# Kernel optimization log

Measured on AMD Instinct MI355X. Metric: run time of the kernel, lower is better.

## Reference

```python
import jax, jax.numpy as jnp
import numpy as np

NUM_USERS = 1_000_000
EMBED = 64
BATCH = 16384
DEG = 50


def setup_inputs() -> dict:
    key = jax.random.key(0)
    ks = jax.random.split(key, 7)
    return {
        "nodes": jax.random.randint(ks[0], (BATCH,), 0, NUM_USERS),
        "neighbors": jax.random.randint(ks[1], (BATCH, DEG), 0, NUM_USERS),
        "u_to_e": jax.random.normal(ks[2], (NUM_USERS, EMBED), jnp.float32) * 0.02,
        "w1": jax.random.normal(ks[3], (2 * EMBED, EMBED), jnp.float32) / np.sqrt(2 * EMBED),
        "b1": jnp.zeros((EMBED,), jnp.float32),
        "w2": jax.random.normal(ks[4], (EMBED, EMBED), jnp.float32) / np.sqrt(EMBED),
        "b2": jnp.zeros((EMBED,), jnp.float32),
        "w3": jax.random.normal(ks[5], (EMBED, 1), jnp.float32) / np.sqrt(EMBED),
        "b3": jnp.zeros((1,), jnp.float32),
    }


def reference(nodes, neighbors, u_to_e, w1, b1, w2, b2, w3, b3):
    # Gather self and neighbor embeddings
    e_u = u_to_e[nodes]            # [B, d]
    e_n = u_to_e[neighbors]        # [B, D, d]
    # GraphRec attention MLP on [neighbor_embed ; self_embed]
    x = jnp.concatenate(
        [e_n, jnp.broadcast_to(e_u[:, None, :], e_n.shape)], axis=-1
    )                              # [B, D, 2d]
    h = jax.nn.relu(x @ w1 + b1)   # [B, D, d]  (dropout is identity in eval)
    h = jax.nn.relu(h @ w2 + b2)   # [B, D, d]
    scores = (h @ w3 + b3)[..., 0] # [B, D]
    att = jax.nn.softmax(scores, axis=1)          # softmax over neighbors
    return jnp.einsum("bd,bde->be", att, e_n)      # attention-weighted neighbor sum [B, d]
```

## Files before the change

### kernel.cpp

```cpp
#include <hip/hip_runtime.h>
#include <hip/hip_bf16.h>
#include <stdint.h>


#define BATCH 16384
#define DEG 50

typedef __attribute__((ext_vector_type(8))) short short8;
typedef __attribute__((ext_vector_type(4))) float f32x4;

__device__ __forceinline__ short bf(float f) {
    __hip_bfloat16 h = __float2bfloat16(f);
    return *reinterpret_cast<short*>(&h);
}
__device__ __forceinline__ unsigned pk2(float a, float b) {
    union { unsigned u; unsigned short s[2]; } v;
    v.s[0] = (unsigned short)bf(a);
    v.s[1] = (unsigned short)bf(b);
    return v.u;
}
__device__ __forceinline__ float bf2f(short s) {
    union { float f; unsigned u; } v;
    v.u = (unsigned)(unsigned short)s << 16;
    return v.f;
}
__device__ __forceinline__ short8 pkrow(f32x4 a, f32x4 c) {
    union { short8 s; unsigned u[4]; } v;
    v.u[0] = pk2(a[0], a[1]); v.u[1] = pk2(a[2], a[3]);
    v.u[2] = pk2(c[0], c[1]); v.u[3] = pk2(c[2], c[3]);
    return v.s;
}
__device__ __forceinline__ short8 cvt_row8(const float* p) {
    f32x4 a = *reinterpret_cast<const f32x4*>(p);
    f32x4 c = *reinterpret_cast<const f32x4*>(p + 4);
    return pkrow(a, c);
}

__global__ void pack_weights(const float* __restrict__ w1, const float* __restrict__ w2,
                             short8* __restrict__ ws) {
    const int f = blockIdx.x;
    const int lane = threadIdx.x;
    const int q = lane >> 4, r = lane & 15;
    const float* w = (f < 16) ? w1 : w2;
    const int g  = (f < 16) ? f : (f - 16);
    const int kt = g >> 2, t = g & 3;
    short8 s;
    #pragma unroll
    for (int j = 0; j < 8; ++j)
        s[j] = bf(w[(32*kt + 8*q + j)*64 + 16*t + r]);
    ws[f*64 + lane] = s;
}

__global__ __launch_bounds__(256, 3)
void graphrec_fused(const int* __restrict__ nodes, const int* __restrict__ neighbors,
                    const float* __restrict__ u_to_e,
                    const short8* __restrict__ wpk,
                    const float* __restrict__ b1, const float* __restrict__ b2,
                    const float* __restrict__ w3,
                    float* __restrict__ out)
{
    __shared__ short8 lds_a[24][64];
    __shared__ int    lds_nbr[4][64];
    __shared__ unsigned short lds_h1[4][1024];
    __shared__ float  lds_stage[4][2][512];

    const int tid  = threadIdx.x;
    const int lane = tid & 63;
    const int wid  = tid >> 6;
    const int q    = lane >> 4;
    const int r    = lane & 15;

    #pragma unroll
    for (int i = 0; i < 6; ++i)
        reinterpret_cast<short8*>(lds_a)[tid + 256*i] = wpk[tid + 256*i];

    const int b    = blockIdx.x * 4 + wid;
    const int node = nodes[b];
    lds_nbr[wid][lane] = (lane < DEG) ? neighbors[b * DEG + lane] : 0;
    __syncthreads();

    int rowv[4];
    #pragma unroll
    for (int mt = 0; mt < 4; ++mt) rowv[mt] = lds_nbr[wid][16*mt + r];

    f32x4 cu[4];
    {
        const float* ub = u_to_e + (size_t)node * 64;
        short8 xu0 = cvt_row8(ub + 8*q);
        short8 xu1 = cvt_row8(ub + 32 + 8*q);
        #pragma unroll
        for (int t = 0; t < 4; ++t) {
            cu[t] = *reinterpret_cast<const f32x4*>(b1 + 16*t + 4*q);
            cu[t] = __builtin_amdgcn_mfma_f32_16x16x32_bf16(lds_a[8  + t][lane], xu0, cu[t], 0, 0, 0);
            cu[t] = __builtin_amdgcn_mfma_f32_16x16x32_bf16(lds_a[12 + t][lane], xu1, cu[t], 0, 0, 0);
        }
    }
    f32x4 b2v[4], w3v[4];
    #pragma unroll
    for (int t = 0; t < 4; ++t) {
        b2v[t] = *reinterpret_cast<const f32x4*>(b2 + 16*t + 4*q);
        w3v[t] = *reinterpret_cast<const f32x4*>(w3 + 16*t + 4*q);
    }

    float* stg = &lds_stage[wid][0][0];
    #define ISSUE_HALF(H) do {                                                           \
        const float* base_ = u_to_e + (size_t)rowv[(H) >> 1] * 64 + 32*((H) & 1) + 4*q;  \
        float* dst_ = stg + ((H) & 1) * 512;                                             \
        _Pragma("unroll")                                                                \
        for (int c_ = 0; c_ < 2; ++c_)                                                   \
            __builtin_amdgcn_global_load_lds(                                            \
                (const __attribute__((address_space(1))) void*)(base_ + 16*c_),          \
                (__attribute__((address_space(3))) void*)(dst_ + 256*c_), 16, 0, 0);     \
    } while (0)

    __builtin_amdgcn_sched_barrier(0);
    ISSUE_HALF(0);
    ISSUE_HALF(1);
    __builtin_amdgcn_sched_barrier(0);

    unsigned short* h1base = lds_h1[wid];
    float agg[16];
    #pragma unroll
    for (int i = 0; i < 16; ++i) agg[i] = 0.f;
    float m_run = -INFINITY, s_run = 0.f;
    const int boff = 256*(q >> 1) + 128*(q & 1) + 4*r;

    #pragma unroll
    for (int mt = 0; mt < 4; ++mt) {
        if (mt < 3) asm volatile("s_waitcnt vmcnt(2)" ::: "memory");
        else        asm volatile("s_waitcnt vmcnt(2)" ::: "memory");
        __builtin_amdgcn_sched_barrier(0);
        f32x4 A  = *reinterpret_cast<const f32x4*>(stg + boff);
        f32x4 Bv = *reinterpret_cast<const f32x4*>(stg + boff + 64);
        short8 xf0 = pkrow(A, Bv);
        if (mt < 3) { ISSUE_HALF(2*mt + 2); }

        if (mt < 3) asm volatile("s_waitcnt vmcnt(2)" ::: "memory");
        else        asm volatile("s_waitcnt vmcnt(0)" ::: "memory");
        __builtin_amdgcn_sched_barrier(0);
        f32x4 C  = *reinterpret_cast<const f32x4*>(stg + 512 + boff);
        f32x4 Dv = *reinterpret_cast<const f32x4*>(stg + 512 + boff + 64);
        short8 xf1 = pkrow(C, Dv);
        if (mt < 3) { ISSUE_HALF(2*mt + 3); }

        f32x4 acc[4] = { cu[0], cu[1], cu[2], cu[3] };
        #pragma unroll
        for (int t = 0; t < 4; ++t) {
            acc[t] = __builtin_amdgcn_mfma_f32_16x16x32_bf16(lds_a[t][lane],     xf0, acc[t], 0, 0, 0);
            acc[t] = __builtin_amdgcn_mfma_f32_16x16x32_bf16(lds_a[4 + t][lane], xf1, acc[t], 0, 0, 0);
        }

        #pragma unroll
        for (int t = 0; t < 4; ++t) {
            unsigned lo = pk2(fmaxf(acc[t][0], 0.f), fmaxf(acc[t][1], 0.f));
            unsigned hi = pk2(fmaxf(acc[t][2], 0.f), fmaxf(acc[t][3], 0.f));
            int off = r * 128 + (((16*t + 4*q) * 2) ^ ((r & 7) << 4));
            *reinterpret_cast<uint2*>((char*)h1base + off) = make_uint2(lo, hi);
        }
        f32x4 acc2[4];
        #pragma unroll
        for (int t2 = 0; t2 < 4; ++t2) acc2[t2] = (f32x4){0.f, 0.f, 0.f, 0.f};
        #pragma unroll
        for (int kt2 = 0; kt2 < 2; ++kt2) {
            int roff = r * 128 + (((32*kt2 + 8*q) * 2) ^ ((r & 7) << 4));
            short8 b2f = *reinterpret_cast<const short8*>((const char*)h1base + roff);
            #pragma unroll
            for (int t2 = 0; t2 < 4; ++t2)
                acc2[t2] = __builtin_amdgcn_mfma_f32_16x16x32_bf16(lds_a[16 + kt2*4 + t2][lane], b2f, acc2[t2], 0, 0, 0);
        }
        float sp = 0.f;
        #pragma unroll
        for (int t2 = 0; t2 < 4; ++t2)
            #pragma unroll
            for (int reg = 0; reg < 4; ++reg)
                sp += fmaxf(acc2[t2][reg] + b2v[t2][reg], 0.f) * w3v[t2][reg];
        sp += __shfl_xor(sp, 16, 64);
        sp += __shfl_xor(sp, 32, 64);

        float v = (mt < 3 || r < 2) ? sp : -INFINITY;
        float tm = v;
        tm = fmaxf(tm, __shfl_xor(tm, 1, 64));
        tm = fmaxf(tm, __shfl_xor(tm, 2, 64));
        tm = fmaxf(tm, __shfl_xor(tm, 4, 64));
        tm = fmaxf(tm, __shfl_xor(tm, 8, 64));
        float m_new = fmaxf(m_run, tm);
        float scale = __expf(m_run - m_new);
        float w = __expf(v - m_new);
        s_run = s_run * scale + w;
        #pragma unroll
        for (int kt = 0; kt < 2; ++kt)
            #pragma unroll
            for (int j = 0; j < 8; ++j) {
                float e = bf2f((kt == 0) ? xf0[j] : xf1[j]);
                agg[kt*8 + j] = fmaf(agg[kt*8 + j], scale, w * e);
            }
        m_run = m_new;
    }
    #undef ISSUE_HALF

    float sum = s_run;
    sum += __shfl_xor(sum, 1, 64);
    sum += __shfl_xor(sum, 2, 64);
    sum += __shfl_xor(sum, 4, 64);
    sum += __shfl_xor(sum, 8, 64);
    float inv = 1.f / sum;
    #pragma unroll
    for (int i = 0; i < 16; ++i) agg[i] *= inv;
    #pragma unroll
    for (int d = 1; d < 16; d <<= 1)
        #pragma unroll
        for (int i = 0; i < 16; ++i)
            agg[i] += __shfl_xor(agg[i], d, 64);

    if (r == 0) {
        float* ob = out + (size_t)b * 64;
        *reinterpret_cast<f32x4*>(ob + 8*q)          = (f32x4){ agg[0],  agg[1],  agg[2],  agg[3]  };
        *reinterpret_cast<f32x4*>(ob + 8*q + 4)      = (f32x4){ agg[4],  agg[5],  agg[6],  agg[7]  };
        *reinterpret_cast<f32x4*>(ob + 32 + 8*q)     = (f32x4){ agg[8],  agg[9],  agg[10], agg[11] };
        *reinterpret_cast<f32x4*>(ob + 32 + 8*q + 4) = (f32x4){ agg[12], agg[13], agg[14], agg[15] };
    }
}

extern "C" void kernel_launch(void* const* d_in, const int* in_sizes, int n_in,
                              void* d_out, int out_size, void* d_ws, size_t ws_size,
                              hipStream_t stream) {
    const int*   nodes     = (const int*)d_in[0];
    const int*   neighbors = (const int*)d_in[1];
    const float* u_to_e    = (const float*)d_in[2];
    const float* w1        = (const float*)d_in[3];
    const float* b1        = (const float*)d_in[4];
    const float* w2        = (const float*)d_in[5];
    const float* b2        = (const float*)d_in[6];
    const float* w3        = (const float*)d_in[7];

    pack_weights<<<dim3(24), dim3(64), 0, stream>>>(w1, w2, (short8*)d_ws);
    graphrec_fused<<<dim3(BATCH / 4), dim3(256), 0, stream>>>(
        nodes, neighbors, u_to_e, (const short8*)d_ws, b1, b2, w3, (float*)d_out);
}
```

Measured before the change: 63.02 us.

## Triple-buffer neighbor staging and drop self-embedding weights from LDS

Neighbor embedding halves are now staged through three LDS slots instead of two, so three global-to-LDS loads are in flight ahead of use rather than two. The wait counts are adjusted to match. To make room, the W1 self-embedding fragments, which are used only once, are read straight from global memory and no longer copied into LDS, shrinking the weight area from 24 to 16 fragments. This deepens memory prefetch to hide gather latency, at the cost of an extra vmcnt(0) wait before the first issues and one-off global weight reads.

```diff
diff --git a/kernel.cpp b/kernel.cpp
--- a/kernel.cpp
+++ b/kernel.cpp
@@ -59,10 +59,10 @@
                     const float* __restrict__ w3,
                     float* __restrict__ out)
 {
-    __shared__ short8 lds_a[24][64];
+    __shared__ short8 lds_a[16][64];
     __shared__ int    lds_nbr[4][64];
     __shared__ unsigned short lds_h1[4][1024];
-    __shared__ float  lds_stage[4][2][512];
+    __shared__ float  lds_stage[4][3][512];
 
     const int tid  = threadIdx.x;
     const int lane = tid & 63;
@@ -71,8 +71,11 @@
     const int r    = lane & 15;
 
     #pragma unroll
-    for (int i = 0; i < 6; ++i)
-        reinterpret_cast<short8*>(lds_a)[tid + 256*i] = wpk[tid + 256*i];
+    for (int i = 0; i < 4; ++i) {
+        const int idx = tid + 256*i;
+        const int f = idx >> 6, l = idx & 63;
+        reinterpret_cast<short8*>(lds_a)[idx] = wpk[((f < 8) ? f : (f + 8))*64 + l];
+    }
 
     const int b    = blockIdx.x * 4 + wid;
     const int node = nodes[b];
@@ -91,8 +94,8 @@
         #pragma unroll
         for (int t = 0; t < 4; ++t) {
             cu[t] = *reinterpret_cast<const f32x4*>(b1 + 16*t + 4*q);
-            cu[t] = __builtin_amdgcn_mfma_f32_16x16x32_bf16(lds_a[8  + t][lane], xu0, cu[t], 0, 0, 0);
-            cu[t] = __builtin_amdgcn_mfma_f32_16x16x32_bf16(lds_a[12 + t][lane], xu1, cu[t], 0, 0, 0);
+            cu[t] = __builtin_amdgcn_mfma_f32_16x16x32_bf16(wpk[(8  + t)*64 + lane], xu0, cu[t], 0, 0, 0);
+            cu[t] = __builtin_amdgcn_mfma_f32_16x16x32_bf16(wpk[(12 + t)*64 + lane], xu1, cu[t], 0, 0, 0);
         }
     }
     f32x4 b2v[4], w3v[4];
@@ -103,19 +106,21 @@
     }
 
     float* stg = &lds_stage[wid][0][0];
-    #define ISSUE_HALF(H) do {                                                           \
-        const float* base_ = u_to_e + (size_t)rowv[(H) >> 1] * 64 + 32*((H) & 1) + 4*q;  \
-        float* dst_ = stg + ((H) & 1) * 512;                                             \
-        _Pragma("unroll")                                                                \
-        for (int c_ = 0; c_ < 2; ++c_)                                                   \
-            __builtin_amdgcn_global_load_lds(                                            \
-                (const __attribute__((address_space(1))) void*)(base_ + 16*c_),          \
-                (__attribute__((address_space(3))) void*)(dst_ + 256*c_), 16, 0, 0);     \
+    #define ISSUE_HALF(H, S) do {                                                       \
+        const float* base_ = u_to_e + (size_t)rowv[(H) >> 1] * 64 + 32*((H) & 1) + 4*q; \
+        float* dst_ = stg + (S) * 512;                                                  \
+        _Pragma("unroll")                                                               \
+        for (int c_ = 0; c_ < 2; ++c_)                                                  \
+            __builtin_amdgcn_global_load_lds(                                           \
+                (const __attribute__((address_space(1))) void*)(base_ + 16*c_),         \
+                (__attribute__((address_space(3))) void*)(dst_ + 256*c_), 16, 0, 0);    \
     } while (0)
 
     __builtin_amdgcn_sched_barrier(0);
-    ISSUE_HALF(0);
-    ISSUE_HALF(1);
+    asm volatile("s_waitcnt vmcnt(0)" ::: "memory");
+    ISSUE_HALF(0, 0);
+    ISSUE_HALF(1, 1);
+    ISSUE_HALF(2, 2);
     __builtin_amdgcn_sched_barrier(0);
 
     unsigned short* h1base = lds_h1[wid];
@@ -127,21 +132,26 @@
 
     #pragma unroll
     for (int mt = 0; mt < 4; ++mt) {
-        if (mt < 3) asm volatile("s_waitcnt vmcnt(2)" ::: "memory");
+        const int h0 = 2*mt, h1 = 2*mt + 1;
+        const int sA = h0 % 3, sB = h1 % 3;
+
+        if (mt < 3) asm volatile("s_waitcnt vmcnt(4)" ::: "memory");
         else        asm volatile("s_waitcnt vmcnt(2)" ::: "memory");
         __builtin_amdgcn_sched_barrier(0);
-        f32x4 A  = *reinterpret_cast<const f32x4*>(stg + boff);
-        f32x4 Bv = *reinterpret_cast<const f32x4*>(stg + boff + 64);
+        f32x4 A  = *reinterpret_cast<const f32x4*>(stg + sA*512 + boff);
+        f32x4 Bv = *reinterpret_cast<const f32x4*>(stg + sA*512 + boff + 64);
         short8 xf0 = pkrow(A, Bv);
-        if (mt < 3) { ISSUE_HALF(2*mt + 2); }
-
-        if (mt < 3) asm volatile("s_waitcnt vmcnt(2)" ::: "memory");
+        __builtin_amdgcn_sched_barrier(0);
+        if (h0 + 3 <= 7) ISSUE_HALF(h0 + 3, (h0 + 3) % 3);
+
+        if (mt < 3) asm volatile("s_waitcnt vmcnt(4)" ::: "memory");
         else        asm volatile("s_waitcnt vmcnt(0)" ::: "memory");
         __builtin_amdgcn_sched_barrier(0);
-        f32x4 C  = *reinterpret_cast<const f32x4*>(stg + 512 + boff);
-        f32x4 Dv = *reinterpret_cast<const f32x4*>(stg + 512 + boff + 64);
+        f32x4 C  = *reinterpret_cast<const f32x4*>(stg + sB*512 + boff);
+        f32x4 Dv = *reinterpret_cast<const f32x4*>(stg + sB*512 + boff + 64);
         short8 xf1 = pkrow(C, Dv);
-        if (mt < 3) { ISSUE_HALF(2*mt + 3); }
+        __builtin_amdgcn_sched_barrier(0);
+        if (h1 + 3 <= 7) ISSUE_HALF(h1 + 3, (h1 + 3) % 3);
 
         f32x4 acc[4] = { cu[0], cu[1], cu[2], cu[3] };
         #pragma unroll
@@ -166,7 +176,7 @@
             short8 b2f = *reinterpret_cast<const short8*>((const char*)h1base + roff);
             #pragma unroll
             for (int t2 = 0; t2 < 4; ++t2)
-                acc2[t2] = __builtin_amdgcn_mfma_f32_16x16x32_bf16(lds_a[16 + kt2*4 + t2][lane], b2f, acc2[t2], 0, 0, 0);
+                acc2[t2] = __builtin_amdgcn_mfma_f32_16x16x32_bf16(lds_a[8 + kt2*4 + t2][lane], b2f, acc2[t2], 0, 0, 0);
         }
         float sp = 0.f;
         #pragma unroll
```

Measured after the change: 64.83 us. 2.9% more time.
